# Kernel optimization log

Measured on AMD Instinct MI355X. Metric: run time of the kernel, lower is better.

The kernel has to match this reference:

```python
import jax, jax.numpy as jnp
import numpy as np

CUTOFF = 10.0
EPS_W = 1e-5
EPS_LN = 1e-5

def _silu(v):
    return v * jax.nn.sigmoid(v)

def setup_inputs() -> dict:
    key = jax.random.key(0)
    ks = jax.random.split(key, 12)
    N, E, H, R = 50000, 300000, 256, 64
    s = lambda fan_in: 1.0 / np.sqrt(fan_in)
    inp = {
        'x': jax.random.normal(ks[0], (N, H), jnp.float32),
        'edge_index': jax.random.randint(ks[1], (2, E), 0, N, jnp.int64 if jax.config.jax_enable_x64 else jnp.int32),
        'distances': jax.random.uniform(ks[2], (E,), jnp.float32) * CUTOFF,
        'centers': jnp.linspace(0.0, CUTOFF, R).astype(jnp.float32),
        'widths': jnp.full((R,), CUTOFF / R, jnp.float32),
        'rbf_w1': jax.random.normal(ks[3], (R, R), jnp.float32) * s(R),
        'rbf_b1': jnp.zeros((R,), jnp.float32),
        'rbf_w2': jax.random.normal(ks[4], (R, R), jnp.float32) * s(R),
        'rbf_b2': jnp.zeros((R,), jnp.float32),
        'filt_w1': jax.random.normal(ks[5], (R, H), jnp.float32) * s(R),
        'filt_b1': jnp.zeros((H,), jnp.float32),
        'filt_w2': jax.random.normal(ks[6], (H, H), jnp.float32) * s(H),
        'filt_b2': jnp.zeros((H,), jnp.float32),
        'filt_w3': jax.random.normal(ks[7], (H, H), jnp.float32) * s(H),
        'filt_b3': jnp.zeros((H,), jnp.float32),
        'node_w': jax.random.normal(ks[8], (H, H), jnp.float32) * s(H),
        'node_b': jnp.zeros((H,), jnp.float32),
        'ln_g': jnp.ones((H,), jnp.float32),
        'ln_b': jnp.zeros((H,), jnp.float32),
        'gate_w': jax.random.normal(ks[9], (H, H), jnp.float32) * s(H),
        'gate_b': jnp.zeros((H,), jnp.float32),
    }
    return inp

def reference(x, edge_index, distances, centers, widths,
              rbf_w1, rbf_b1, rbf_w2, rbf_b2,
              filt_w1, filt_b1, filt_w2, filt_b2, filt_w3, filt_b3,
              node_w, node_b, ln_g, ln_b, gate_w, gate_b):
    # LearnableRBF: envelope * gaussian basis, then 2-layer SiLU proj
    d = distances
    env = 0.5 * (jnp.cos(d * jnp.pi / CUTOFF) + 1.0) * (d < CUTOFF).astype(x.dtype)  # [E]
    rbf = jnp.exp(-0.5 * ((d[:, None] - centers) / (jnp.abs(widths) + EPS_W)) ** 2)   # [E,R]
    r = rbf * env[:, None]
    r = _silu(r @ rbf_w1 + rbf_b1) @ rbf_w2 + rbf_b2                                  # [E,R]
    # filter network: Lin-SiLU-Lin-SiLU-Lin
    W = _silu(r @ filt_w1 + filt_b1)
    W = _silu(W @ filt_w2 + filt_b2) @ filt_w3 + filt_b3                              # [E,H]
    # gather -> modulate -> scatter-add (CFConv messaging)
    row, col = edge_index[0], edge_index[1]
    msg = (x[col] @ node_w + node_b) * W                                              # [E,H]
    agg = jax.ops.segment_sum(msg, row, num_segments=x.shape[0])                      # [N,H]
    h = x + agg
    mu = jnp.mean(h, axis=-1, keepdims=True)
    var = jnp.var(h, axis=-1, keepdims=True)
    out = (h - mu) / jnp.sqrt(var + EPS_LN) * ln_g + ln_b
    return out * jax.nn.sigmoid(out @ gate_w + gate_b)
```

## Files before the change

### kernel.cpp

```cpp
#include <hip/hip_runtime.h>
#include <hip/hip_bf16.h>
#include <math.h>

typedef __attribute__((ext_vector_type(8))) short bf16x8;
typedef __attribute__((ext_vector_type(4))) float f32x4;
typedef unsigned short ushort_t;

constexpr float F_CUTOFF = 10.0f;
constexpr float F_EPS_W  = 1e-5f;
constexpr float F_EPS_LN = 1e-5f;
constexpr float F_PI     = 3.14159265358979323846f;

__device__ __forceinline__ float silu_f(float v)   { return v / (1.0f + __expf(-v)); }
__device__ __forceinline__ float sigmoid_f(float v){ return 1.0f / (1.0f + __expf(-v)); }

__device__ __forceinline__ ushort_t f2bf(float f) {
    union { __hip_bfloat16 h; ushort_t u; } v; v.h = __float2bfloat16(f); return v.u;
}
__device__ __forceinline__ float bf2f(ushort_t u) {
    union { __hip_bfloat16 h; ushort_t u; } v; v.u = u; return __bfloat162float(v.h);
}

__device__ __forceinline__ float f4c(const float4& v, int q) {
    return q == 0 ? v.x : q == 1 ? v.y : q == 2 ? v.z : v.w;
}

__global__ void cvt_transpose_kernel(const float* __restrict__ in, ushort_t* __restrict__ out,
                                     int K, int N, int logK)
{
    int idx = blockIdx.x * 256 + threadIdx.x;
    if (idx >= K * N) return;
    int n = idx >> logK;
    int k = idx & (K - 1);
    out[idx] = f2bf(in[k * N + n]);
}

__global__ void combine_w_kernel(const float* __restrict__ w2, const float* __restrict__ fw1,
                                 ushort_t* __restrict__ out)
{
    int idx = blockIdx.x * 256 + threadIdx.x;
    int c = idx >> 6, j = idx & 63;
    float s = 0.f;
    #pragma unroll 8
    for (int n = 0; n < 64; ++n) s += w2[j * 64 + n] * fw1[n * 256 + c];
    out[idx] = f2bf(s);
}

__global__ void combine_b_kernel(const float* __restrict__ b2, const float* __restrict__ fw1,
                                 const float* __restrict__ fb1, float* __restrict__ out)
{
    int c = threadIdx.x;
    float s = fb1[c];
    #pragma unroll 8
    for (int n = 0; n < 64; ++n) s += b2[n] * fw1[n * 256 + c];
    out[c] = s;
}

__global__ __launch_bounds__(256)
void gemm256_bf16_kernel(const float* __restrict__ A, const float* __restrict__ Wm,
                         const float* __restrict__ bias, ushort_t* __restrict__ out, int M)
{
    __shared__ float4 As4[64][64];
    const int t = threadIdx.x;
    const int row0 = blockIdx.x * 64;

    #pragma unroll
    for (int i = 0; i < 16; ++i) {
        int flat = t + i * 256;
        int r = flat >> 6, k4 = flat & 63;
        int row = row0 + r;
        float4 v = make_float4(0.f, 0.f, 0.f, 0.f);
        if (row < M) v = reinterpret_cast<const float4*>(A)[row * 64 + k4];
        As4[r][k4] = v;
    }
    __syncthreads();

    const int jt  = t & 31;
    const int et  = t >> 5;
    const int j04 = jt * 2;
    const int r0  = et * 8;

    float acc[8][8];
    #pragma unroll
    for (int r = 0; r < 8; ++r)
        #pragma unroll
        for (int c = 0; c < 8; ++c) acc[r][c] = 0.f;

    for (int k4 = 0; k4 < 64; ++k4) {
        float4 a4[8];
        #pragma unroll
        for (int r = 0; r < 8; ++r) a4[r] = As4[r0 + r][k4];
        #pragma unroll
        for (int q = 0; q < 4; ++q) {
            const int k = k4 * 4 + q;
            float4 b0 = reinterpret_cast<const float4*>(Wm)[k * 64 + j04];
            float4 b1 = reinterpret_cast<const float4*>(Wm)[k * 64 + j04 + 1];
            float bb[8] = {b0.x, b0.y, b0.z, b0.w, b1.x, b1.y, b1.z, b1.w};
            #pragma unroll
            for (int r = 0; r < 8; ++r) {
                float av = f4c(a4[r], q);
                #pragma unroll
                for (int c = 0; c < 8; ++c) acc[r][c] = fmaf(av, bb[c], acc[r][c]);
            }
        }
    }

    float4 bv0 = reinterpret_cast<const float4*>(bias)[j04];
    float4 bv1 = reinterpret_cast<const float4*>(bias)[j04 + 1];
    float bb[8] = {bv0.x, bv0.y, bv0.z, bv0.w, bv1.x, bv1.y, bv1.z, bv1.w};

    #pragma unroll
    for (int r = 0; r < 8; ++r) {
        int row = row0 + r0 + r;
        if (row >= M) continue;
        ushort_t o8[8];
        #pragma unroll
        for (int c = 0; c < 8; ++c) o8[c] = f2bf(acc[r][c] + bb[c]);
        *reinterpret_cast<uint4*>(out + (size_t)row * 256 + jt * 8) = *reinterpret_cast<uint4*>(o8);
    }
}

__global__ __launch_bounds__(256)
void gate_gemm_kernel(const float* __restrict__ A, const float* __restrict__ Wm,
                      const float* __restrict__ bias, float* __restrict__ out, int M)
{
    __shared__ float4 As4[64][64];
    const int t = threadIdx.x;
    const int row0 = blockIdx.x * 64;

    #pragma unroll
    for (int i = 0; i < 16; ++i) {
        int flat = t + i * 256;
        int r = flat >> 6, k4 = flat & 63;
        int row = row0 + r;
        float4 v = make_float4(0.f, 0.f, 0.f, 0.f);
        if (row < M) v = reinterpret_cast<const float4*>(A)[row * 64 + k4];
        As4[r][k4] = v;
    }
    __syncthreads();

    const int jt  = t & 31;
    const int et  = t >> 5;
    const int j04 = jt * 2;
    const int r0  = et * 8;

    float acc[8][8];
    #pragma unroll
    for (int r = 0; r < 8; ++r)
        #pragma unroll
        for (int c = 0; c < 8; ++c) acc[r][c] = 0.f;

    for (int k4 = 0; k4 < 64; ++k4) {
        float4 a4[8];
        #pragma unroll
        for (int r = 0; r < 8; ++r) a4[r] = As4[r0 + r][k4];
        #pragma unroll
        for (int q = 0; q < 4; ++q) {
            const int k = k4 * 4 + q;
            float4 b0 = reinterpret_cast<const float4*>(Wm)[k * 64 + j04];
            float4 b1 = reinterpret_cast<const float4*>(Wm)[k * 64 + j04 + 1];
            float bb[8] = {b0.x, b0.y, b0.z, b0.w, b1.x, b1.y, b1.z, b1.w};
            #pragma unroll
            for (int r = 0; r < 8; ++r) {
                float av = f4c(a4[r], q);
                #pragma unroll
                for (int c = 0; c < 8; ++c) acc[r][c] = fmaf(av, bb[c], acc[r][c]);
            }
        }
    }

    float4 bv0 = reinterpret_cast<const float4*>(bias)[j04];
    float4 bv1 = reinterpret_cast<const float4*>(bias)[j04 + 1];
    float bb[8] = {bv0.x, bv0.y, bv0.z, bv0.w, bv1.x, bv1.y, bv1.z, bv1.w};

    #pragma unroll
    for (int r = 0; r < 8; ++r) {
        int row = row0 + r0 + r;
        if (row >= M) continue;
        float4 a0 = As4[r0 + r][j04];
        float4 a1 = As4[r0 + r][j04 + 1];
        float aa[8] = {a0.x, a0.y, a0.z, a0.w, a1.x, a1.y, a1.z, a1.w};
        float o[8];
        #pragma unroll
        for (int c = 0; c < 8; ++c) o[c] = aa[c] * sigmoid_f(acc[r][c] + bb[c]);
        reinterpret_cast<float4*>(out)[row * 64 + j04]     = make_float4(o[0], o[1], o[2], o[3]);
        reinterpret_cast<float4*>(out)[row * 64 + j04 + 1] = make_float4(o[4], o[5], o[6], o[7]);
    }
}

template<int KS, int NT, bool SILU>
__device__ __forceinline__ void mlp_stage(const unsigned char* in, unsigned char* out,
                                          const ushort_t* __restrict__ Wt,
                                          const float* __restrict__ bias,
                                          int wn, int g, int q)
{
    constexpr int K = KS * 32;
    f32x4 acc[2][NT];
    #pragma unroll
    for (int mt = 0; mt < 2; ++mt)
        #pragma unroll
        for (int nt = 0; nt < NT; ++nt) acc[mt][nt] = (f32x4){0.f, 0.f, 0.f, 0.f};

    #pragma unroll
    for (int kk = 0; kk < KS; ++kk) {
        bf16x8 b[NT];
        #pragma unroll
        for (int nt = 0; nt < NT; ++nt) {
            int n = (wn * NT + nt) * 16 + q;
            b[nt] = *reinterpret_cast<const bf16x8*>(Wt + n * K + kk * 32 + g * 8);
        }
        bf16x8 a[2];
        #pragma unroll
        for (int mt = 0; mt < 2; ++mt) {
            int m = mt * 16 + q;
            int unit = (4 * kk + g) ^ (m & 7);
            a[mt] = *reinterpret_cast<const bf16x8*>(in + m * 512 + unit * 16);
        }
        #pragma unroll
        for (int mt = 0; mt < 2; ++mt)
            #pragma unroll
            for (int nt = 0; nt < NT; ++nt)
                acc[mt][nt] = __builtin_amdgcn_mfma_f32_16x16x32_bf16(a[mt], b[nt], acc[mt][nt], 0, 0, 0);
    }

    const bool evenq = (q & 1) == 0;
    #pragma unroll
    for (int nt = 0; nt < NT; ++nt) {
        int n0  = (wn * NT + nt) * 16 + q;
        int n_e = n0 & ~1;
        float2 bv = *reinterpret_cast<const float2*>(bias + n_e);
        #pragma unroll
        for (int mt = 0; mt < 2; ++mt) {
            float v[4], p[4];
            #pragma unroll
            for (int r = 0; r < 4; ++r) { v[r] = acc[mt][nt][r]; p[r] = __shfl_xor(v[r], 1, 64); }
            #pragma unroll
            for (int rr = 0; rr < 2; ++rr) {
                int r = evenq ? rr : (2 + rr);
                float lo = (evenq ? v[r] : p[r]) + bv.x;
                float hi = (evenq ? p[r] : v[r]) + bv.y;
                if (SILU) { lo = silu_f(lo); hi = silu_f(hi); }
                int m = mt * 16 + 4 * g + r;
                unsigned u = (unsigned)f2bf(lo) | ((unsigned)f2bf(hi) << 16);
                int byte = m * 512 + (((n_e >> 3) ^ (m & 7)) << 4) + ((n_e & 7) * 2);
                *reinterpret_cast<unsigned*>(out + byte) = u;
            }
        }
    }
}

__global__ __launch_bounds__(256, 4)
void edge_mfma_kernel(const float* __restrict__ dist, const int* __restrict__ eidx,
                      const float* __restrict__ centers, const float* __restrict__ widths,
                      const ushort_t* __restrict__ wt_rbf1, const float* __restrict__ rbf_b1,
                      const ushort_t* __restrict__ wt_comb, const float* __restrict__ b_comb,
                      const ushort_t* __restrict__ wt_f2, const float* __restrict__ filt_b2,
                      const ushort_t* __restrict__ wt_f3, const float* __restrict__ filt_b3,
                      const ushort_t* __restrict__ y, float* __restrict__ agg, int E)
{
    __shared__ __align__(16) unsigned char bufA[16384];
    __shared__ __align__(16) unsigned char bufB[16384];

    const int t  = threadIdx.x;
    const int e0 = blockIdx.x * 32;
    const int wn   = t >> 6;
    const int lane = t & 63;
    const int g = lane >> 4, q = lane & 15;

    const int e_own  = t >> 3;
    const int chunk  = t & 7;
    const int ge_own = e0 + e_own;
    const int col_own = (ge_own < E) ? eidx[E + ge_own] : 0;
    uint4 yv[4];
    #pragma unroll
    for (int i = 0; i < 4; ++i)
        yv[i] = *reinterpret_cast<const uint4*>(y + (size_t)col_own * 256 + (i * 8 + chunk) * 8);

    {
        float d = (ge_own < E) ? dist[ge_own] : F_CUTOFF;
        float env = (d < F_CUTOFF) ? 0.5f * (__cosf(d * (F_PI / F_CUTOFF)) + 1.0f) : 0.0f;
        unsigned char* rowp = bufA + e_own * 512;
        int k0 = chunk * 8;
        #pragma unroll
        for (int i = 0; i < 4; ++i) {
            int n = k0 + 2 * i;
            float c0 = centers[n],     w0 = fabsf(widths[n]) + F_EPS_W;
            float c1 = centers[n + 1], w1 = fabsf(widths[n + 1]) + F_EPS_W;
            float z0 = (d - c0) / w0, z1 = (d - c1) / w1;
            float r0 = env * __expf(-0.5f * z0 * z0);
            float r1 = env * __expf(-0.5f * z1 * z1);
            unsigned u = (unsigned)f2bf(r0) | ((unsigned)f2bf(r1) << 16);
            int byte = (((n >> 3) ^ (e_own & 7)) << 4) + ((n & 7) * 2);
            *reinterpret_cast<unsigned*>(rowp + byte) = u;
        }
    }
    __syncthreads();

    mlp_stage<2, 1, true>(bufA, bufB, wt_rbf1, rbf_b1, wn, g, q);
    __syncthreads();
    mlp_stage<2, 4, true>(bufB, bufA, wt_comb, b_comb, wn, g, q);
    __syncthreads();
    mlp_stage<8, 4, true>(bufA, bufB, wt_f2, filt_b2, wn, g, q);
    __syncthreads();

    #pragma unroll
    for (int i = 0; i < 4; ++i)
        *reinterpret_cast<uint4*>(bufA + e_own * 512 + (i * 8 + chunk) * 16) = yv[i];
    __syncthreads();

    {
        f32x4 acc[2][4];
        #pragma unroll
        for (int mt = 0; mt < 2; ++mt)
            #pragma unroll
            for (int nt = 0; nt < 4; ++nt) acc[mt][nt] = (f32x4){0.f, 0.f, 0.f, 0.f};

        #pragma unroll
        for (int kk = 0; kk < 8; ++kk) {
            bf16x8 b[4];
            #pragma unroll
            for (int nt = 0; nt < 4; ++nt) {
                int n = (wn * 4 + nt) * 16 + q;
                b[nt] = *reinterpret_cast<const bf16x8*>(wt_f3 + n * 256 + kk * 32 + g * 8);
            }
            bf16x8 a[2];
            #pragma unroll
            for (int mt = 0; mt < 2; ++mt) {
                int m = mt * 16 + q;
                int unit = (4 * kk + g) ^ (m & 7);
                a[mt] = *reinterpret_cast<const bf16x8*>(bufB + m * 512 + unit * 16);
            }
            #pragma unroll
            for (int mt = 0; mt < 2; ++mt)
                #pragma unroll
                for (int nt = 0; nt < 4; ++nt)
                    acc[mt][nt] = __builtin_amdgcn_mfma_f32_16x16x32_bf16(a[mt], b[nt], acc[mt][nt], 0, 0, 0);
        }

        float bn[4];
        int   nn[4];
        #pragma unroll
        for (int nt = 0; nt < 4; ++nt) { nn[nt] = (wn * 4 + nt) * 16 + q; bn[nt] = filt_b3[nn[nt]]; }

        #pragma unroll
        for (int mt = 0; mt < 2; ++mt) {
            #pragma unroll
            for (int r = 0; r < 4; ++r) {
                int m  = mt * 16 + 4 * g + r;
                int ge = e0 + m;
                if (ge < E) {
                    int rowi = eidx[ge];
                    float* arow = agg + (size_t)rowi * 256;
                    const unsigned char* yrow = bufA + m * 512;
                    #pragma unroll
                    for (int nt = 0; nt < 4; ++nt) {
                        float wv = acc[mt][nt][r] + bn[nt];
                        float yvv = bf2f(*reinterpret_cast<const ushort_t*>(yrow + nn[nt] * 2));
                        unsafeAtomicAdd(&arow[nn[nt]], wv * yvv);
                    }
                }
            }
        }
    }
}

__global__ __launch_bounds__(256)
void ln_kernel(const float* __restrict__ x, const float* __restrict__ agg,
               const float* __restrict__ g, const float* __restrict__ b,
               float* __restrict__ out0, int N)
{
    int lane = threadIdx.x & 63;
    int row  = blockIdx.x * 4 + (threadIdx.x >> 6);
    if (row >= N) return;
    float4 hx = reinterpret_cast<const float4*>(x)[row * 64 + lane];
    float4 ha = reinterpret_cast<const float4*>(agg)[row * 64 + lane];
    float4 h  = make_float4(hx.x + ha.x, hx.y + ha.y, hx.z + ha.z, hx.w + ha.w);
    float s  = h.x + h.y + h.z + h.w;
    float s2 = h.x * h.x + h.y * h.y + h.z * h.z + h.w * h.w;
    #pragma unroll
    for (int off = 32; off > 0; off >>= 1) {
        s  += __shfl_xor(s,  off, 64);
        s2 += __shfl_xor(s2, off, 64);
    }
    float mu  = s * (1.0f / 256.0f);
    float var = s2 * (1.0f / 256.0f) - mu * mu;
    float inv = rsqrtf(var + F_EPS_LN);
    float4 gv = reinterpret_cast<const float4*>(g)[lane];
    float4 bv = reinterpret_cast<const float4*>(b)[lane];
    float4 o;
    o.x = (h.x - mu) * inv * gv.x + bv.x;
    o.y = (h.y - mu) * inv * gv.y + bv.y;
    o.z = (h.z - mu) * inv * gv.z + bv.z;
    o.w = (h.w - mu) * inv * gv.w + bv.w;
    reinterpret_cast<float4*>(out0)[row * 64 + lane] = o;
}

extern "C" void kernel_launch(void* const* d_in, const int* in_sizes, int n_in,
                              void* d_out, int out_size, void* d_ws, size_t ws_size,
                              hipStream_t stream)
{
    const float* x       = (const float*)d_in[0];
    const int*   eidx    = (const int*)  d_in[1];
    const float* dist    = (const float*)d_in[2];
    const float* centers = (const float*)d_in[3];
    const float* widths  = (const float*)d_in[4];
    const float* rbf_w1  = (const float*)d_in[5];
    const float* rbf_b1  = (const float*)d_in[6];
    const float* rbf_w2  = (const float*)d_in[7];
    const float* rbf_b2  = (const float*)d_in[8];
    const float* filt_w1 = (const float*)d_in[9];
    const float* filt_b1 = (const float*)d_in[10];
    const float* filt_w2 = (const float*)d_in[11];
    const float* filt_b2 = (const float*)d_in[12];
    const float* filt_w3 = (const float*)d_in[13];
    const float* filt_b3 = (const float*)d_in[14];
    const float* node_w  = (const float*)d_in[15];
    const float* node_b  = (const float*)d_in[16];
    const float* ln_g    = (const float*)d_in[17];
    const float* ln_b    = (const float*)d_in[18];
    const float* gate_w  = (const float*)d_in[19];
    const float* gate_b  = (const float*)d_in[20];

    const int N = in_sizes[0] / 256;
    const int E = in_sizes[2];

    ushort_t* y_bf   = (ushort_t*)d_ws;
    ushort_t* wt1    = y_bf + (size_t)N * 256;
    ushort_t* wcomb  = wt1 + 64 * 64;
    ushort_t* wf2    = wcomb + 256 * 64;
    ushort_t* wf3    = wf2 + 256 * 256;
    float*    bcomb  = (float*)(wf3 + 256 * 256);

    float* agg = (float*)d_out;

    hipMemsetAsync(d_out, 0, (size_t)out_size * sizeof(float), stream);

    cvt_transpose_kernel<<<dim3((64 * 64 + 255) / 256),   256, 0, stream>>>(rbf_w1,  wt1, 64, 64, 6);
    combine_w_kernel<<<dim3(64), 256, 0, stream>>>(rbf_w2, filt_w1, wcomb);
    combine_b_kernel<<<dim3(1), 256, 0, stream>>>(rbf_b2, filt_w1, filt_b1, bcomb);
    cvt_transpose_kernel<<<dim3((256 * 256 + 255) / 256), 256, 0, stream>>>(filt_w2, wf2, 256, 256, 8);
    cvt_transpose_kernel<<<dim3((256 * 256 + 255) / 256), 256, 0, stream>>>(filt_w3, wf3, 256, 256, 8);

    gemm256_bf16_kernel<<<dim3((N + 63) / 64), 256, 0, stream>>>(x, node_w, node_b, y_bf, N);

    edge_mfma_kernel<<<dim3((E + 31) / 32), 256, 0, stream>>>(
        dist, eidx, centers, widths,
        wt1, rbf_b1, wcomb, bcomb,
        wf2, filt_b2, wf3, filt_b3,
        y_bf, agg, E);

    ln_kernel<<<dim3((N + 3) / 4), 256, 0, stream>>>(x, agg, ln_g, ln_b, (float*)d_out, N);
    gate_gemm_kernel<<<dim3((N + 63) / 64), 256, 0, stream>>>((float*)d_out, gate_w, gate_b, (float*)d_out, N);
}
```

Baseline: 824.4 us.

## Replace atomic scatter-add with CSR-sorted message buffer and segmented reduction

Builds a CSR layout of edges by destination row (count, single-block scan, slot scatter), then has the edge kernel write each message row to its sorted slot instead of issuing float atomics into agg. A fused agg+LayerNorm kernel sums each node's contiguous message rows and applies LN. This removes the contention and traffic of 77M float atomics, at the cost of writing and re-reading a ~300MB fp32 message buffer plus extra preprocessing kernels, including a serial single-block scan. Falls back to the atomic path when the workspace is too small.

```diff
diff --git a/kernel.cpp b/kernel.cpp
--- a/kernel.cpp
+++ b/kernel.cpp
@@ -23,6 +23,52 @@
 
 __device__ __forceinline__ float f4c(const float4& v, int q) {
     return q == 0 ? v.x : q == 1 ? v.y : q == 2 ? v.z : v.w;
+}
+
+__global__ void count_kernel(const int* __restrict__ eidx, int* __restrict__ cnt, int E)
+{
+    int e = blockIdx.x * 256 + threadIdx.x;
+    if (e < E) atomicAdd(&cnt[eidx[e]], 1);
+}
+
+__global__ __launch_bounds__(1024)
+void scan_kernel(const int* __restrict__ cnt, int* __restrict__ start,
+                 int* __restrict__ cursor, int N)
+{
+    __shared__ int part[1024];
+    const int tid = threadIdx.x;
+    const int C = (N + 1023) >> 10;
+    const int base = tid * C;
+    int s = 0;
+    for (int i = 0; i < C; ++i) {
+        int idx = base + i;
+        if (idx < N) s += cnt[idx];
+    }
+    part[tid] = s;
+    __syncthreads();
+    for (int off = 1; off < 1024; off <<= 1) {
+        int v = (tid >= off) ? part[tid - off] : 0;
+        __syncthreads();
+        part[tid] += v;
+        __syncthreads();
+    }
+    int run = part[tid] - s;
+    for (int i = 0; i < C; ++i) {
+        int idx = base + i;
+        if (idx < N) {
+            start[idx]  = run;
+            cursor[idx] = run;
+            run += cnt[idx];
+        }
+    }
+    if (tid == 1023) start[N] = part[1023];
+}
+
+__global__ void scatter_kernel(const int* __restrict__ eidx, int* __restrict__ cursor,
+                               int* __restrict__ slot, int E)
+{
+    int e = blockIdx.x * 256 + threadIdx.x;
+    if (e < E) slot[e] = atomicAdd(&cursor[eidx[e]], 1);
 }
 
 __global__ void cvt_transpose_kernel(const float* __restrict__ in, ushort_t* __restrict__ out,
@@ -249,6 +295,7 @@
     }
 }
 
+template<int TWO>
 __global__ __launch_bounds__(256, 4)
 void edge_mfma_kernel(const float* __restrict__ dist, const int* __restrict__ eidx,
                       const float* __restrict__ centers, const float* __restrict__ widths,
@@ -256,16 +303,24 @@
                       const ushort_t* __restrict__ wt_comb, const float* __restrict__ b_comb,
                       const ushort_t* __restrict__ wt_f2, const float* __restrict__ filt_b2,
                       const ushort_t* __restrict__ wt_f3, const float* __restrict__ filt_b3,
-                      const ushort_t* __restrict__ y, float* __restrict__ agg, int E)
+                      const ushort_t* __restrict__ y, const int* __restrict__ slot,
+                      float* __restrict__ dst, int E)
 {
     __shared__ __align__(16) unsigned char bufA[16384];
     __shared__ __align__(16) unsigned char bufB[16384];
+    __shared__ int rs_s[32];
 
     const int t  = threadIdx.x;
     const int e0 = blockIdx.x * 32;
     const int wn   = t >> 6;
     const int lane = t & 63;
     const int g = lane >> 4, q = lane & 15;
+
+    if (t < 32) {
+        int ge = e0 + t;
+        if (TWO) rs_s[t] = (ge < E) ? slot[ge] : 0;
+        else     rs_s[t] = (ge < E) ? eidx[ge] : 0;
+    }
 
     const int e_own  = t >> 3;
     const int chunk  = t & 7;
@@ -349,19 +404,63 @@
                 int m  = mt * 16 + 4 * g + r;
                 int ge = e0 + m;
                 if (ge < E) {
-                    int rowi = eidx[ge];
-                    float* arow = agg + (size_t)rowi * 256;
                     const unsigned char* yrow = bufA + m * 512;
-                    #pragma unroll
-                    for (int nt = 0; nt < 4; ++nt) {
-                        float wv = acc[mt][nt][r] + bn[nt];
-                        float yvv = bf2f(*reinterpret_cast<const ushort_t*>(yrow + nn[nt] * 2));
-                        unsafeAtomicAdd(&arow[nn[nt]], wv * yvv);
+                    if (TWO) {
+                        float* mrow = dst + (size_t)rs_s[m] * 256;
+                        #pragma unroll
+                        for (int nt = 0; nt < 4; ++nt) {
+                            float wv = acc[mt][nt][r] + bn[nt];
+                            float yvv = bf2f(*reinterpret_cast<const ushort_t*>(yrow + nn[nt] * 2));
+                            mrow[nn[nt]] = wv * yvv;
+                        }
+                    } else {
+                        float* arow = dst + (size_t)rs_s[m] * 256;
+                        #pragma unroll
+                        for (int nt = 0; nt < 4; ++nt) {
+                            float wv = acc[mt][nt][r] + bn[nt];
+                            float yvv = bf2f(*reinterpret_cast<const ushort_t*>(yrow + nn[nt] * 2));
+                            unsafeAtomicAdd(&arow[nn[nt]], wv * yvv);
+                        }
                     }
                 }
             }
         }
     }
+}
+
+__global__ __launch_bounds__(256)
+void agg_ln_kernel(const float* __restrict__ x, const float* __restrict__ msg,
+                   const int* __restrict__ start,
+                   const float* __restrict__ g, const float* __restrict__ b,
+                   float* __restrict__ out0, int N)
+{
+    int lane = threadIdx.x & 63;
+    int row  = blockIdx.x * 4 + (threadIdx.x >> 6);
+    if (row >= N) return;
+    int s0 = start[row], s1 = start[row + 1];
+    float4 h = reinterpret_cast<const float4*>(x)[row * 64 + lane];
+    for (int s = s0; s < s1; ++s) {
+        float4 m = reinterpret_cast<const float4*>(msg)[(size_t)s * 64 + lane];
+        h.x += m.x; h.y += m.y; h.z += m.z; h.w += m.w;
+    }
+    float su  = h.x + h.y + h.z + h.w;
+    float s2 = h.x * h.x + h.y * h.y + h.z * h.z + h.w * h.w;
+    #pragma unroll
+    for (int off = 32; off > 0; off >>= 1) {
+        su += __shfl_xor(su, off, 64);
+        s2 += __shfl_xor(s2, off, 64);
+    }
+    float mu  = su * (1.0f / 256.0f);
+    float var = s2 * (1.0f / 256.0f) - mu * mu;
+    float inv = rsqrtf(var + F_EPS_LN);
+    float4 gv = reinterpret_cast<const float4*>(g)[lane];
+    float4 bv = reinterpret_cast<const float4*>(b)[lane];
+    float4 o;
+    o.x = (h.x - mu) * inv * gv.x + bv.x;
+    o.y = (h.y - mu) * inv * gv.y + bv.y;
+    o.z = (h.z - mu) * inv * gv.z + bv.z;
+    o.w = (h.w - mu) * inv * gv.w + bv.w;
+    reinterpret_cast<float4*>(out0)[row * 64 + lane] = o;
 }
 
 __global__ __launch_bounds__(256)
@@ -424,31 +523,59 @@
     const int N = in_sizes[0] / 256;
     const int E = in_sizes[2];
 
-    ushort_t* y_bf   = (ushort_t*)d_ws;
-    ushort_t* wt1    = y_bf + (size_t)N * 256;
-    ushort_t* wcomb  = wt1 + 64 * 64;
-    ushort_t* wf2    = wcomb + 256 * 64;
-    ushort_t* wf3    = wf2 + 256 * 256;
-    float*    bcomb  = (float*)(wf3 + 256 * 256);
-
-    float* agg = (float*)d_out;
-
-    hipMemsetAsync(d_out, 0, (size_t)out_size * sizeof(float), stream);
-
-    cvt_transpose_kernel<<<dim3((64 * 64 + 255) / 256),   256, 0, stream>>>(rbf_w1,  wt1, 64, 64, 6);
-    combine_w_kernel<<<dim3(64), 256, 0, stream>>>(rbf_w2, filt_w1, wcomb);
-    combine_b_kernel<<<dim3(1), 256, 0, stream>>>(rbf_b2, filt_w1, filt_b1, bcomb);
-    cvt_transpose_kernel<<<dim3((256 * 256 + 255) / 256), 256, 0, stream>>>(filt_w2, wf2, 256, 256, 8);
-    cvt_transpose_kernel<<<dim3((256 * 256 + 255) / 256), 256, 0, stream>>>(filt_w3, wf3, 256, 256, 8);
-
-    gemm256_bf16_kernel<<<dim3((N + 63) / 64), 256, 0, stream>>>(x, node_w, node_b, y_bf, N);
-
-    edge_mfma_kernel<<<dim3((E + 31) / 32), 256, 0, stream>>>(
-        dist, eidx, centers, widths,
-        wt1, rbf_b1, wcomb, bcomb,
-        wf2, filt_b2, wf3, filt_b3,
-        y_bf, agg, E);
-
-    ln_kernel<<<dim3((N + 3) / 4), 256, 0, stream>>>(x, agg, ln_g, ln_b, (float*)d_out, N);
-    gate_gemm_kernel<<<dim3((N + 63) / 64), 256, 0, stream>>>((float*)d_out, gate_w, gate_b, (float*)d_out, N);
-}
+    char* wsb = (char*)d_ws;
+    size_t off = 0;
+    auto alloc = [&](size_t bytes, size_t align) -> char* {
+        off = (off + align - 1) & ~(align - 1);
+        char* p = wsb + off;
+        off += bytes;
+        return p;
+    };
+    ushort_t* y_bf  = (ushort_t*)alloc((size_t)N * 256 * 2, 16);
+    ushort_t* wt1   = (ushort_t*)alloc(64 * 64 * 2, 16);
+    ushort_t* wcomb = (ushort_t*)alloc(256 * 64 * 2, 16);
+    ushort_t* wf2   = (ushort_t*)alloc(256 * 256 * 2, 16);
+    ushort_t* wf3   = (ushort_t*)alloc(256 * 256 * 2, 16);
+    float*    bcomb = (float*)   alloc(256 * 4, 16);
+    int*      cnt   = (int*)     alloc((size_t)N * 4, 16);
+    int*      start = (int*)     alloc(((size_t)N + 1) * 4, 16);
+    int*      cursor= (int*)     alloc((size_t)N * 4, 16);
+    int*      slot  = (int*)     alloc((size_t)E * 4, 16);
+    float*    msg   = (float*)   alloc((size_t)E * 256 * 4, 1024);
+    const bool two_phase = (off <= ws_size);
+
+    dim3 b256(256);
+
+    cvt_transpose_kernel<<<dim3((64 * 64 + 255) / 256),   b256, 0, stream>>>(rbf_w1,  wt1, 64, 64, 6);
+    combine_w_kernel<<<dim3(64), b256, 0, stream>>>(rbf_w2, filt_w1, wcomb);
+    combine_b_kernel<<<dim3(1), b256, 0, stream>>>(rbf_b2, filt_w1, filt_b1, bcomb);
+    cvt_transpose_kernel<<<dim3((256 * 256 + 255) / 256), b256, 0, stream>>>(filt_w2, wf2, 256, 256, 8);
+    cvt_transpose_kernel<<<dim3((256 * 256 + 255) / 256), b256, 0, stream>>>(filt_w3, wf3, 256, 256, 8);
+
+    gemm256_bf16_kernel<<<dim3((N + 63) / 64), b256, 0, stream>>>(x, node_w, node_b, y_bf, N);
+
+    if (two_phase) {
+        hipMemsetAsync(cnt, 0, (size_t)N * 4, stream);
+        count_kernel<<<dim3((E + 255) / 256), b256, 0, stream>>>(eidx, cnt, E);
+        scan_kernel<<<dim3(1), 1024, 0, stream>>>(cnt, start, cursor, N);
+        scatter_kernel<<<dim3((E + 255) / 256), b256, 0, stream>>>(eidx, cursor, slot, E);
+
+        edge_mfma_kernel<1><<<dim3((E + 31) / 32), b256, 0, stream>>>(
+            dist, eidx, centers, widths,
+            wt1, rbf_b1, wcomb, bcomb,
+            wf2, filt_b2, wf3, filt_b3,
+            y_bf, slot, msg, E);
+
+        agg_ln_kernel<<<dim3((N + 3) / 4), b256, 0, stream>>>(x, msg, start, ln_g, ln_b, (float*)d_out, N);
+    } else {
+        hipMemsetAsync(d_out, 0, (size_t)out_size * sizeof(float), stream);
+        edge_mfma_kernel<0><<<dim3((E + 31) / 32), b256, 0, stream>>>(
+            dist, eidx, centers, widths,
+            wt1, rbf_b1, wcomb, bcomb,
+            wf2, filt_b2, wf3, filt_b3,
+            y_bf, slot, (float*)d_out, E);
+        ln_kernel<<<dim3((N + 3) / 4), b256, 0, stream>>>(x, (float*)d_out, ln_g, ln_b, (float*)d_out, N);
+    }
+
+    gate_gemm_kernel<<<dim3((N + 63) / 64), b256, 0, stream>>>((float*)d_out, gate_w, gate_b, (float*)d_out, N);
+}
```

Result: no change. 822.8 us (-0.2%).
